# Optimization experiments

Hardware: AMD Instinct MI355X
Metric: run time of the kernel (lower is better)

## Reference

```python
import jax, jax.numpy as jnp
import numpy as np
from jax import lax

H = 512  # out_size (hidden)

def lstm_layer(x, W_ih, W_hh, b_ih, b_hh):
    # x: [B, T, F] -> hidden sequence [B, T, H]; matches torch.nn.LSTMCell math
    B = x.shape[0]
    h0 = jnp.zeros((B, H), dtype=x.dtype)
    c0 = jnp.zeros((B, H), dtype=x.dtype)

    def step(carry, x_t):
        h, c = carry
        gates = x_t @ W_ih.T + b_ih + h @ W_hh.T + b_hh  # [B, 4H], gate order i,f,g,o
        i, f, g, o = jnp.split(gates, 4, axis=-1)
        i = jax.nn.sigmoid(i)
        f = jax.nn.sigmoid(f)
        g = jnp.tanh(g)
        o = jax.nn.sigmoid(o)
        c_new = f * c + i * g
        h_new = o * jnp.tanh(c_new)
        return (h_new, c_new), h_new

    xt = jnp.swapaxes(x, 0, 1)  # [T, B, F]
    (_, _), hs = lax.scan(step, (h0, c0), xt)
    return jnp.swapaxes(hs, 0, 1)  # [B, T, H]


def setup_inputs() -> dict:
    key = jax.random.key(0)
    ks = jax.random.split(key, 9)
    B, T, F = 64, 512, 256
    s = 1.0 / np.sqrt(H)  # torch LSTMCell init scale
    inp = {
        "x": jax.random.normal(ks[0], (B, T, F), dtype=jnp.float32),
        "W_ih0": jax.random.uniform(ks[1], (4 * H, F), jnp.float32, -s, s),
        "W_hh0": jax.random.uniform(ks[2], (4 * H, H), jnp.float32, -s, s),
        "b_ih0": jax.random.uniform(ks[3], (4 * H,), jnp.float32, -s, s),
        "b_hh0": jax.random.uniform(ks[4], (4 * H,), jnp.float32, -s, s),
        "W_ih1": jax.random.uniform(ks[5], (4 * H, H), jnp.float32, -s, s),
        "W_hh1": jax.random.uniform(ks[6], (4 * H, H), jnp.float32, -s, s),
        "b_ih1": jax.random.uniform(ks[7], (4 * H,), jnp.float32, -s, s),
        "b_hh1": jax.random.uniform(ks[8], (4 * H,), jnp.float32, -s, s),
    }
    return inp


def reference(x, W_ih0, W_hh0, b_ih0, b_hh0, W_ih1, W_hh1, b_ih1, b_hh1):
    # Layer 0 (in_size -> H), dropout=0.0 is identity; layer 1 (H -> H)
    a = lstm_layer(x, W_ih0, W_hh0, b_ih0, b_hh0)
    a = lstm_layer(a, W_ih1, W_hh1, b_ih1, b_hh1)
    return a  # yhat: [B, T, H]; final_state is (a[:, -1], c_T) in the original
```

## Files before the change

kernel.cpp:

```cpp
#include <hip/hip_runtime.h>
#include <math.h>


#define TT 512
#define FF 256
#define HH 512
#define NB 256

typedef __attribute__((ext_vector_type(4)))  float f32x4;
typedef __attribute__((ext_vector_type(8)))  short short8;
typedef __attribute__((ext_vector_type(16))) short short16;

__device__ __forceinline__ float sigmoidf_(float v){ return 1.0f/(1.0f+__expf(-v)); }

__device__ __forceinline__ unsigned short f2bf(float f){
    unsigned u = __float_as_uint(f);
    u += 0x7FFFu + ((u>>16)&1u);
    return (unsigned short)(u>>16);
}
__device__ __forceinline__ float bf2f(unsigned short h){ return __uint_as_float(((unsigned)h)<<16); }

__device__ __forceinline__ unsigned long long ld8coh(const unsigned* p){
    return __hip_atomic_load((const unsigned long long*)p, __ATOMIC_RELAXED, __HIP_MEMORY_SCOPE_AGENT);
}
__device__ __forceinline__ int ld4coh(const int* p){
    return __hip_atomic_load(p, __ATOMIC_RELAXED, __HIP_MEMORY_SCOPE_AGENT);
}
__device__ __forceinline__ void st4coh(unsigned* p, unsigned v){
    __hip_atomic_store(p, v, __ATOMIC_RELAXED, __HIP_MEMORY_SCOPE_AGENT);
}
__device__ __forceinline__ void stslot(int* p, int v){
    __hip_atomic_store(p, v, __ATOMIC_RELAXED, __HIP_MEMORY_SCOPE_AGENT);
}

union HU { unsigned long long q[4]; short16 v; };

__device__ __forceinline__ void split8(const float* v, short8& h8, short8& l8){
#pragma unroll
    for (int j=0;j<8;++j){
        const unsigned short hh = f2bf(v[j]);
        h8[j] = (short)hh;
        l8[j] = (short)f2bf(v[j]-bf2f(hh));
    }
}

__device__ __forceinline__ void loadsplit(const float* p, short8& h8, short8& l8){
    float v[8];
#pragma unroll
    for (int j=0;j<8;++j) v[j]=p[j];
    split8(v, h8, l8);
}

#define MFMA(a,b,c) __builtin_amdgcn_mfma_f32_16x16x32_bf16((a),(b),(c),0,0,0)

struct SMem { float part[8][16][66]; };

template<int LAYER>
__device__ __forceinline__ void run(
    const float* __restrict__ x,
    const float* __restrict__ WA, const float* __restrict__ WB,
    const float* __restrict__ bi, const float* __restrict__ bh,
    unsigned* __restrict__ hp0, unsigned* __restrict__ hp1,
    float* __restrict__ out, int* __restrict__ slots,
    const int bg, const int tile_u, SMem* sm)
{
    const int tid  = threadIdx.x;
    const int lane = tid & 63;
    const int wv   = __builtin_amdgcn_readfirstlane(tid>>6);
    const int nn   = lane & 15;
    const int quad = lane >> 4;
    const int bglob= bg*16 + nn;

    constexpr int NC = (LAYER==0) ? 3 : 4;
    short8 wHi[4][NC], wLo[4][NC];
#pragma unroll
    for (int nt=0;nt<4;++nt){
        const int jg = ((nn>>2)<<9) + (tile_u<<4) + (nt<<2) + (nn&3);
        if (LAYER==0){
            const float* rA = WA + (size_t)jg*FF;
            const float* rB = WB + (size_t)jg*HH;
            loadsplit(rA + wv*32 + quad*8, wHi[nt][0], wLo[nt][0]);
#pragma unroll
            for (int c=0;c<2;++c)
                loadsplit(rB + (2*wv+c)*32 + quad*8, wHi[nt][1+c], wLo[nt][1+c]);
        } else {
            const float* rw = ((wv<4) ? WA : WB) + (size_t)jg*HH;
#pragma unroll
            for (int c=0;c<4;++c)
                loadsplit(rw + ((wv&3)*4+c)*32 + quad*8, wHi[nt][c], wLo[nt][c]);
        }
    }

    const int b_e = tid>>4, ul = tid&15;
    const int u_e = (tile_u<<4) + ul;
    float br[4]={0.f,0.f,0.f,0.f}; float creg=0.f;
    if (tid<256){
#pragma unroll
        for (int g=0; g<4; ++g) br[g] = bi[(g<<9)+u_e] + bh[(g<<9)+u_e];
    }

    const int myslot = bg*64 + LAYER*32 + tile_u;
    const f32x4 Z = {0.f,0.f,0.f,0.f};

#define LOADH(U, OCT) { \
        const unsigned* p_ = src + ((size_t)((OCT))*64 + bglob)*8; \
        U.q[0]=ld8coh(p_);   U.q[1]=ld8coh(p_+2); \
        U.q[2]=ld8coh(p_+4); U.q[3]=ld8coh(p_+6); }

#define MATHH(U, SLOT) { \
        const short8 aH = __builtin_shufflevector(U.v,U.v,0,2,4,6,8,10,12,14); \
        const short8 aL = __builtin_shufflevector(U.v,U.v,1,3,5,7,9,11,13,15); \
        _Pragma("unroll") \
        for (int nt=0;nt<4;++nt){ \
            accH[nt]=MFMA(aH,wHi[nt][(SLOT)],accH[nt]); \
            accM[nt]=MFMA(aH,wLo[nt][(SLOT)],accM[nt]); \
            accM[nt]=MFMA(aL,wHi[nt][(SLOT)],accM[nt]); \
        } }

    for (int s=0; s<=TT; ++s){
        const bool active = LAYER ? (s>0) : (s<TT);
        const int t = LAYER ? (s-1) : s;
        f32x4 accH[4], accM[4];
#pragma unroll
        for (int nt=0;nt<4;++nt){ accH[nt]=Z; accM[nt]=Z; }

        if (LAYER==0 && active){
            const float* p = x + ((size_t)bglob*TT + t)*FF + wv*32 + quad*8;
            float v[8];
            const float4 a0 = *(const float4*)(p);
            const float4 a1 = *(const float4*)(p+4);
            v[0]=a0.x; v[1]=a0.y; v[2]=a0.z; v[3]=a0.w;
            v[4]=a1.x; v[5]=a1.y; v[6]=a1.z; v[7]=a1.w;
            short8 aH, aL; split8(v, aH, aL);
#pragma unroll
            for (int nt=0;nt<4;++nt){
                accH[nt]=MFMA(aH,wHi[nt][0],accH[nt]);
                accM[nt]=MFMA(aH,wLo[nt][0],accM[nt]);
                accM[nt]=MFMA(aL,wHi[nt][0],accM[nt]);
            }
        }

        if (wv==0){
            if (LAYER==0){
                const int* sp = slots + bg*64 + (lane&31);
                while (!__all(ld4coh(sp) >= s)) __builtin_amdgcn_s_sleep(1);
            } else {
                const int* sp = slots + bg*64 + lane;
                while (!__all(ld4coh(sp) >= s)) __builtin_amdgcn_s_sleep(1);
            }
        }
        __syncthreads();

        if (active){
            if (LAYER==0){
                const unsigned* src = hp0 + ((s+3)&3)*32768;
                HU u0,u1;
                LOADH(u0,(2*wv+0)*4+quad);
                LOADH(u1,(2*wv+1)*4+quad);
                MATHH(u0,1); MATHH(u1,2);
            } else {
                const unsigned* src = (wv<4) ? hp0 + ((s+3)&3)*32768
                                             : hp1 + (s&1)*32768;
                HU u0,u1,u2,u3;
                LOADH(u0,((wv&3)*4+0)*4+quad);
                LOADH(u1,((wv&3)*4+1)*4+quad);
                LOADH(u2,((wv&3)*4+2)*4+quad);
                LOADH(u3,((wv&3)*4+3)*4+quad);
                MATHH(u0,0); MATHH(u1,1); MATHH(u2,2); MATHH(u3,3);
            }

#pragma unroll
            for (int nt=0;nt<4;++nt)
#pragma unroll
                for (int r=0;r<4;++r)
                    sm->part[wv][quad*4+r][nt*16+nn] = accH[nt][r]+accM[nt][r];
        }

        if (LAYER==0 && wv==0){
            const int* sp2 = slots + bg*64 + 32 + (lane&31);
            while (!__all(ld4coh(sp2) >= s-2)) __builtin_amdgcn_s_sleep(1);
        }
        __syncthreads();

        if (active && tid<256){
            float pre[4];
#pragma unroll
            for (int g=0; g<4; ++g){
                const int col = ((ul>>2)<<4) + (g<<2) + (ul&3);
                float sum = br[g];
#pragma unroll
                for (int w=0;w<8;++w) sum += sm->part[w][b_e][col];
                pre[g]=sum;
            }
            const float iv = sigmoidf_(pre[0]);
            const float fv = sigmoidf_(pre[1]);
            const float gv = tanhf(pre[2]);
            const float ov = sigmoidf_(pre[3]);
            creg = fv*creg + iv*gv;
            const float hn = ov * tanhf(creg);
            const unsigned short hh = f2bf(hn);
            const unsigned short hl = f2bf(hn - bf2f(hh));
            const unsigned pk = ((unsigned)hl<<16) | (unsigned)hh;
            const int bge = bg*16 + b_e;
            const int idx = ((u_e>>3)*64 + bge)*8 + (u_e&7);
            if (LAYER==0) st4coh(hp0 + (s&3)*32768 + idx, pk);
            else {
                st4coh(hp1 + ((s+1)&1)*32768 + idx, pk);
                out[((size_t)bge*TT + t)*HH + u_e] = hn;
            }
        }

        __syncthreads();
        if (tid==0) stslot(slots + myslot, s+1);
    }
#undef LOADH
#undef MATHH
}

__global__ void __launch_bounds__(512,1) lstm_persist(
    const float* __restrict__ x,
    const float* __restrict__ Wih0, const float* __restrict__ Whh0,
    const float* __restrict__ bi0,  const float* __restrict__ bh0,
    const float* __restrict__ Wih1, const float* __restrict__ Whh1,
    const float* __restrict__ bi1,  const float* __restrict__ bh1,
    unsigned* hp0, unsigned* hp1, float* out, int* slots)
{
    __shared__ SMem sm;
    const int layer = blockIdx.x>>7, lid = blockIdx.x&127;
    const int bg = lid>>5, tile_u = lid&31;
    if (layer==0) run<0>(x, Wih0, Whh0, bi0, bh0, hp0, hp1, out, slots, bg, tile_u, &sm);
    else          run<1>(x, Wih1, Whh1, bi1, bh1, hp0, hp1, out, slots, bg, tile_u, &sm);
}

extern "C" void kernel_launch(void* const* d_in, const int* in_sizes, int n_in,
                              void* d_out, int out_size, void* d_ws, size_t ws_size,
                              hipStream_t stream) {
    (void)in_sizes; (void)n_in; (void)out_size; (void)ws_size;
    const float* x    = (const float*)d_in[0];
    const float* Wih0 = (const float*)d_in[1];
    const float* Whh0 = (const float*)d_in[2];
    const float* bi0  = (const float*)d_in[3];
    const float* bh0  = (const float*)d_in[4];
    const float* Wih1 = (const float*)d_in[5];
    const float* Whh1 = (const float*)d_in[6];
    const float* bi1  = (const float*)d_in[7];
    const float* bh1  = (const float*)d_in[8];
    float* out = (float*)d_out;
    unsigned* ws = (unsigned*)d_ws;

    unsigned* hp0 = ws;
    unsigned* hp1 = ws + 4*32768;
    int* slots    = (int*)(ws + 6*32768);

    hipMemsetAsync(d_ws, 0, (6*32768 + 256)*sizeof(unsigned), stream);

    void* args[] = {
        (void*)&x, (void*)&Wih0, (void*)&Whh0, (void*)&bi0, (void*)&bh0,
        (void*)&Wih1, (void*)&Whh1, (void*)&bi1, (void*)&bh1,
        (void*)&hp0, (void*)&hp1, (void*)&out, (void*)&slots
    };
    hipLaunchCooperativeKernel((const void*)lstm_persist, dim3(NB), dim3(512),
                               args, 0, stream);
}
```

Measured before the change: 2.459 ms.

## Replace end-of-step block barrier with per-wave completion tokens

```diff
diff --git a/kernel.cpp b/kernel.cpp
--- a/kernel.cpp
+++ b/kernel.cpp
@@ -23,9 +23,6 @@
 __device__ __forceinline__ unsigned long long ld8coh(const unsigned* p){
     return __hip_atomic_load((const unsigned long long*)p, __ATOMIC_RELAXED, __HIP_MEMORY_SCOPE_AGENT);
 }
-__device__ __forceinline__ int ld4coh(const int* p){
-    return __hip_atomic_load(p, __ATOMIC_RELAXED, __HIP_MEMORY_SCOPE_AGENT);
-}
 __device__ __forceinline__ void st4coh(unsigned* p, unsigned v){
     __hip_atomic_store(p, v, __ATOMIC_RELAXED, __HIP_MEMORY_SCOPE_AGENT);
 }
@@ -34,6 +31,7 @@
 }
 
 union HU { unsigned long long q[4]; short16 v; };
+union SL { unsigned long long q; int i[2]; };
 
 __device__ __forceinline__ void split8(const float* v, short8& h8, short8& l8){
 #pragma unroll
@@ -53,7 +51,7 @@
 
 #define MFMA(a,b,c) __builtin_amdgcn_mfma_f32_16x16x32_bf16((a),(b),(c),0,0,0)
 
-struct SMem { float part[8][16][66]; };
+struct SMem { float part[8][16][68]; };
 
 template<int LAYER>
 __device__ __forceinline__ void run(
@@ -99,7 +97,8 @@
         for (int g=0; g<4; ++g) br[g] = bi[(g<<9)+u_e] + bh[(g<<9)+u_e];
     }
 
-    const int myslot = bg*64 + LAYER*32 + tile_u;
+    int* const sb = slots + bg*256;
+    int* const mytok = sb + LAYER*128 + tile_u*4 + wv;
     const f32x4 Z = {0.f,0.f,0.f,0.f};
 
 #define LOADH(U, OCT) { \
@@ -142,11 +141,21 @@
 
         if (wv==0){
             if (LAYER==0){
-                const int* sp = slots + bg*64 + (lane&31);
-                while (!__all(ld4coh(sp) >= s)) __builtin_amdgcn_s_sleep(1);
+                const int* sp = sb + 2*lane;
+                for(;;){
+                    SL a; a.q = ld8coh((const unsigned*)sp);
+                    if (__all((a.i[0]>=s)&(a.i[1]>=s))) break;
+                    __builtin_amdgcn_s_sleep(1);
+                }
             } else {
-                const int* sp = slots + bg*64 + lane;
-                while (!__all(ld4coh(sp) >= s)) __builtin_amdgcn_s_sleep(1);
+                const int* sp0 = sb + 2*lane;
+                const int* sp1 = sb + 128 + 2*lane;
+                for(;;){
+                    SL a,b; a.q = ld8coh((const unsigned*)sp0);
+                    b.q = ld8coh((const unsigned*)sp1);
+                    if (__all((a.i[0]>=s)&(a.i[1]>=s)&(b.i[0]>=s)&(b.i[1]>=s))) break;
+                    __builtin_amdgcn_s_sleep(1);
+                }
             }
         }
         __syncthreads();
@@ -177,8 +186,12 @@
         }
 
         if (LAYER==0 && wv==0){
-            const int* sp2 = slots + bg*64 + 32 + (lane&31);
-            while (!__all(ld4coh(sp2) >= s-2)) __builtin_amdgcn_s_sleep(1);
+            const int* sp2 = sb + 128 + 2*lane;
+            for(;;){
+                SL a; a.q = ld8coh((const unsigned*)sp2);
+                if (__all((a.i[0]>=s-2)&(a.i[1]>=s-2))) break;
+                __builtin_amdgcn_s_sleep(1);
+            }
         }
         __syncthreads();
 
@@ -210,8 +223,10 @@
             }
         }
 
-        __syncthreads();
-        if (tid==0) stslot(slots + myslot, s+1);
+        if (wv < 4){
+            asm volatile("s_waitcnt vmcnt(0)" ::: "memory");
+            if (lane==0) stslot(mytok, s+1);
+        }
     }
 #undef LOADH
 #undef MATHH
@@ -252,7 +267,7 @@
     unsigned* hp1 = ws + 4*32768;
     int* slots    = (int*)(ws + 6*32768);
 
-    hipMemsetAsync(d_ws, 0, (6*32768 + 256)*sizeof(unsigned), stream);
+    hipMemsetAsync(d_ws, 0, (6*32768 + 1024)*sizeof(unsigned), stream);
 
     void* args[] = {
         (void*)&x, (void*)&Wih0, (void*)&Whh0, (void*)&bi0, (void*)&bh0,
```

Measured after the change: 4.012 ms. +63.2%, slower.
